# Optimization experiments

Measured on AMD Instinct MI355X. Metric: run time of the kernel, lower is better.

The kernel has to match this reference:

```python
import jax, jax.numpy as jnp
import numpy as np


def _conv2d_same(x, w, b):
    # x: [B,H,W,Cin], w: [kh,kw,Cin,Cout] (Keras HWIO), b: [Cout]
    y = jax.lax.conv_general_dilated(
        x, w, window_strides=(1, 1), padding='SAME',
        dimension_numbers=('NHWC', 'HWIO', 'NHWC'))
    return y + b


def _bilateral_slice_apply(grid, guide, image):
    # HDRNet bilateral_slice_apply with has_offset=True.
    # grid:  [B, gh, gw, gd, (ci+1)*co]
    # guide: [B, H, W] in [0,1]
    # image: [B, H, W, ci]
    B, gh, gw, gd, nc = grid.shape
    _, H, W, ci = image.shape
    co = nc // (ci + 1)
    dt = grid.dtype

    # Continuous grid coordinates (HDRNet convention: pixel centers, -0.5 shift)
    gx = (jnp.arange(W, dtype=dt) + 0.5) * gw / W - 0.5          # [W]
    gy = (jnp.arange(H, dtype=dt) + 0.5) * gh / H - 0.5          # [H]
    gz = guide.astype(dt) * gd - 0.5                             # [B,H,W]

    fx = jnp.floor(gx)
    fy = jnp.floor(gy)
    fz = jnp.floor(gz)
    bidx = jnp.arange(B)[:, None, None]                          # [B,1,1]

    coeffs = jnp.zeros((B, H, W, nc), dtype=dt)
    for dz in (0, 1):
        zz = fz + dz
        wz = jnp.maximum(1.0 - jnp.abs(gz - zz), 0.0)            # [B,H,W]
        zi = jnp.clip(zz.astype(jnp.int32), 0, gd - 1)           # [B,H,W]
        for dy in (0, 1):
            yy = fy + dy
            wy = jnp.maximum(1.0 - jnp.abs(gy - yy), 0.0)        # [H]
            yi = jnp.clip(yy.astype(jnp.int32), 0, gh - 1)       # [H]
            for dx in (0, 1):
                xx = fx + dx
                wx = jnp.maximum(1.0 - jnp.abs(gx - xx), 0.0)    # [W]
                xi = jnp.clip(xx.astype(jnp.int32), 0, gw - 1)   # [W]
                corner = grid[bidx, yi[None, :, None], xi[None, None, :], zi]  # [B,H,W,nc]
                w = wz * wy[None, :, None] * wx[None, None, :]   # [B,H,W]
                coeffs = coeffs + corner * w[..., None]

    # Per-pixel affine transform: coeffs -> [B,H,W,co,ci+1]
    A = coeffs.reshape(B, H, W, co, ci + 1)
    return jnp.einsum('bhwoi,bhwi->bhwo', A[..., :ci], image) + A[..., ci]


def setup_inputs() -> dict:
    key = jax.random.key(0)
    k1, k2, k3, k4 = jax.random.split(key, 4)
    B, H, W = 4, 1024, 1024
    grid = jax.random.normal(k1, (B, 16, 16, 8, 12), dtype=jnp.float32)
    guide = jax.random.uniform(k2, (B, H, W), dtype=jnp.float32)
    image = jax.random.normal(k3, (B, H, W, 3), dtype=jnp.float32)
    conv_w = jax.random.normal(k4, (3, 3, 3, 3), dtype=jnp.float32) * 0.1
    conv_b = jnp.zeros((3,), dtype=jnp.float32)
    return {'grid': grid, 'guide': guide, 'image': image,
            'conv_w': conv_w, 'conv_b': conv_b}


def reference(grid, guide, image, conv_w, conv_b):
    x = _conv2d_same(image, conv_w, conv_b)
    return _bilateral_slice_apply(grid, guide, x)
```

## Files before the change

### kernel.cpp

```cpp
#include <hip/hip_runtime.h>

#define H_  1024
#define W_  1024
#define B_  4
#define GH  16
#define GW  16
#define GD  8
#define NC  12
#define CELLF (GD * NC)
#define YROWF (GW * CELLF)

#define TW 64
#define TH 8

typedef _Float16 h2 __attribute__((ext_vector_type(2)));

__device__ __forceinline__ h2 u2h(unsigned int u) { return __builtin_bit_cast(h2, u); }

template<bool G>
__device__ __forceinline__ void load3g(const float* base, int yy, int xx, float* d) {
    if constexpr (!G) {
        __builtin_memcpy(d, base + (yy * W_ + xx) * 3, 12);
    } else {
        d[0] = 0.f; d[1] = 0.f; d[2] = 0.f;
        if (((unsigned)yy < (unsigned)H_) && ((unsigned)xx < (unsigned)W_))
            __builtin_memcpy(d, base + (yy * W_ + xx) * 3, 12);
    }
}

template<bool G>
__device__ __forceinline__ void loadrow9(const float* base, int ry, int x, float* d) {
    load3g<G>(base, ry, x - 1, d + 0);
    load3g<G>(base, ry, x,     d + 3);
    load3g<G>(base, ry, x + 1, d + 6);
}

__device__ __forceinline__ void conv3r(const float* a, const float* b, const float* c,
                                       float* acc, const float* wgt,
                                       float bias0, float bias1, float bias2) {
    acc[0] = bias0; acc[1] = bias1; acc[2] = bias2;
    const float* rows[3] = {a, b, c};
    #pragma unroll
    for (int kh = 0; kh < 3; ++kh)
        #pragma unroll
        for (int kw = 0; kw < 3; ++kw)
            #pragma unroll
            for (int ci = 0; ci < 3; ++ci) {
                float v = rows[kh][kw * 3 + ci];
                const float* wb = wgt + ((kh * 3 + kw) * 3 + ci) * 3;
                acc[0] += v * wb[0];
                acc[1] += v * wb[1];
                acc[2] += v * wb[2];
            }
}

__global__ __launch_bounds__(256, 8)
void fused_conv_slice(const float* __restrict__ grid,
                      const float* __restrict__ guide,
                      const float* __restrict__ image,
                      const float* __restrict__ conv_w,
                      const float* __restrict__ conv_b,
                      float* __restrict__ out)
{
    __shared__ uint4 s_t128[TH][3 * GD];
    __shared__ uint2 s_t64[TH][3 * GD];

    const int tx  = threadIdx.x;
    const int tyq = threadIdx.y;
    const int bx  = blockIdx.x;
    const int by  = blockIdx.y;
    const int b   = blockIdx.z;
    const int x0 = bx * TW;
    const int y0 = by * TH;
    const int tid = tyq * 64 + tx;
    const float* ib = image + b * (H_ * W_ * 3);

    int cells[3];
    cells[0] = max(bx - 1, 0);
    cells[1] = bx;
    cells[2] = min(bx + 1, GW - 1);
    const float* gB = grid + b * (GH * GW * GD * NC);
    {
        int rr = tid >> 5;
        int le = tid & 31;
        int y  = y0 + rr;
        float gyf = (y + 0.5f) * (1.0f / 64.0f) - 0.5f;
        float fyf = floorf(gyf);
        float tyw = gyf - fyf;
        int iy = (int)fyf;
        int yi0 = min(max(iy, 0), GH - 1);
        int yi1 = min(max(iy + 1, 0), GH - 1);
        float wy0 = 1.0f - tyw, wy1 = tyw;
        const float4* G0 = (const float4*)(gB + yi0 * YROWF);
        const float4* G1 = (const float4*)(gB + yi1 * YROWF);
        #pragma unroll
        for (int k = 0; k < 3; ++k) {
            int e = le + k * 32;
            if (e < 72) {
                int s  = (e >= 48) ? 2 : ((e >= 24) ? 1 : 0);
                int re = e - s * 24;
                int z  = re / 3;
                int c4 = re - z * 3;
                int off = cells[s] * 24 + re;
                float4 v0 = G0[off], v1 = G1[off];
                h2 p0, p1;
                p0.x = (_Float16)(wy0 * v0.x + wy1 * v1.x);
                p0.y = (_Float16)(wy0 * v0.y + wy1 * v1.y);
                p1.x = (_Float16)(wy0 * v0.z + wy1 * v1.z);
                p1.y = (_Float16)(wy0 * v0.w + wy1 * v1.w);
                uint2 u;
                u.x = __builtin_bit_cast(unsigned int, p0);
                u.y = __builtin_bit_cast(unsigned int, p1);
                int ci = s * GD + z;
                unsigned short* dst = (c4 == 2)
                    ? (unsigned short*)&s_t64[rr][ci]
                    : (unsigned short*)&s_t128[rr][ci] + c4 * 4;
                *(uint2*)dst = u;
            }
        }
    }

    const int x = x0 + tx;
    const int lr = tyq * 2;
    const int guidebase = b * (H_ * W_);
    float g2[2];
    #pragma unroll
    for (int j = 0; j < 2; ++j)
        g2[j] = guide[guidebase + (y0 + lr + j) * W_ + x];

    float wgt[81];
    #pragma unroll
    for (int i = 0; i < 81; ++i) wgt[i] = conv_w[i];
    float bias0 = conv_b[0], bias1 = conv_b[1], bias2 = conv_b[2];

    const int R0 = y0 + lr;
    float ra[9], rb[9], rc[9], rd[9];
    const bool edge = (bx == 0) | (bx == (W_ / TW - 1)) |
                      (by == 0) | (by == (H_ / TH - 1));
    if (!edge) {
        loadrow9<false>(ib, R0 - 1, x, ra);
        loadrow9<false>(ib, R0 + 0, x, rb);
        loadrow9<false>(ib, R0 + 1, x, rc);
        loadrow9<false>(ib, R0 + 2, x, rd);
    } else {
        loadrow9<true>(ib, R0 - 1, x, ra);
        loadrow9<true>(ib, R0 + 0, x, rb);
        loadrow9<true>(ib, R0 + 1, x, rc);
        loadrow9<true>(ib, R0 + 2, x, rd);
    }
    float acc2r[2][3];
    conv3r(ra, rb, rc, acc2r[0], wgt, bias0, bias1, bias2);
    conv3r(rb, rc, rd, acc2r[1], wgt, bias0, bias1, bias2);

    __syncthreads();

    float gxf = (x + 0.5f) * (1.0f / 64.0f) - 0.5f;
    float fxf = floorf(gxf);
    float txw = gxf - fxf;
    float wxa = 1.0f - txw, wxb = txw;
    int s0 = (int)fxf - (bx - 1);

    const int outbase = b * (H_ * W_ * 3);

    #pragma unroll
    for (int j = 0; j < 2; ++j) {
        int y = y0 + lr + j;
        const uint4* T128 = &s_t128[lr + j][0];
        const uint2* T64  = &s_t64[lr + j][0];

        float gzf = g2[j] * 8.0f - 0.5f;
        float fzf = floorf(gzf);
        float tz = gzf - fzf;
        int iz = (int)fzf;
        int zb = min(max(iz, 0), GD - 2);
        float wA = (iz < 0) ? 1.0f : ((iz > GD - 2) ? 0.0f : (1.0f - tz));
        float wB = 1.0f - wA;

        float m0 = wxa * wA, m1 = wxa * wB, m2 = wxb * wA, m3 = wxb * wB;
        h2 m0h = {(_Float16)m0, (_Float16)m0};
        h2 m1h = {(_Float16)m1, (_Float16)m1};
        h2 m2h = {(_Float16)m2, (_Float16)m2};
        h2 m3h = {(_Float16)m3, (_Float16)m3};

        int ci0 = s0 * GD + zb;
        uint4 Alo = T128[ci0];          uint2 Ahi = T64[ci0];
        uint4 Blo = T128[ci0 + 1];      uint2 Bhi = T64[ci0 + 1];
        uint4 Clo = T128[ci0 + GD];     uint2 Chi = T64[ci0 + GD];
        uint4 Dlo = T128[ci0 + GD + 1]; uint2 Dhi = T64[ci0 + GD + 1];

        h2 A[6]  = {u2h(Alo.x), u2h(Alo.y), u2h(Alo.z), u2h(Alo.w), u2h(Ahi.x), u2h(Ahi.y)};
        h2 Bv[6] = {u2h(Blo.x), u2h(Blo.y), u2h(Blo.z), u2h(Blo.w), u2h(Bhi.x), u2h(Bhi.y)};
        h2 Cv[6] = {u2h(Clo.x), u2h(Clo.y), u2h(Clo.z), u2h(Clo.w), u2h(Chi.x), u2h(Chi.y)};
        h2 Dv[6] = {u2h(Dlo.x), u2h(Dlo.y), u2h(Dlo.z), u2h(Dlo.w), u2h(Dhi.x), u2h(Dhi.y)};

        h2 c[6];
        #pragma unroll
        for (int k = 0; k < 6; ++k)
            c[k] = __builtin_elementwise_fma(A[k], m0h,
                   __builtin_elementwise_fma(Bv[k], m1h,
                   __builtin_elementwise_fma(Cv[k], m2h, Dv[k] * m3h)));

        float a0 = acc2r[j][0], a1 = acc2r[j][1], a2 = acc2r[j][2];
        h2 q01 = {(_Float16)a0, (_Float16)a1};
        h2 q21 = {(_Float16)a2, (_Float16)1.0f};

        int oidx = outbase + (y * W_ + x) * 3;
        #pragma unroll
        for (int o3 = 0; o3 < 3; ++o3) {
            float t = __builtin_amdgcn_fdot2(c[2 * o3 + 1], q21, 0.0f, false);
            out[oidx + o3] = __builtin_amdgcn_fdot2(c[2 * o3], q01, t, false);
        }
    }
}

extern "C" void kernel_launch(void* const* d_in, const int* in_sizes, int n_in,
                              void* d_out, int out_size, void* d_ws, size_t ws_size,
                              hipStream_t stream) {
    const float* grid   = (const float*)d_in[0];
    const float* guide  = (const float*)d_in[1];
    const float* image  = (const float*)d_in[2];
    const float* conv_w = (const float*)d_in[3];
    const float* conv_b = (const float*)d_in[4];
    float* out = (float*)d_out;

    dim3 block(64, 4, 1);
    dim3 grid_dim(W_ / TW, H_ / TH, B_);
    fused_conv_slice<<<grid_dim, block, 0, stream>>>(grid, guide, image, conv_w, conv_b, out);
}
```

Before: 146.9 us.

## Stage image halo into LDS via async global_load_lds and drop block barrier

Each wave now copies its 4-row by 66-pixel image halo into a per-wave shared buffer. Interior tiles use coalesced dword global_load_lds transfers that go straight to LDS. Edge tiles use guarded loads and LDS stores. The 3x3 conv then reads its rows from LDS instead of issuing many overlapping unaligned 12-byte global loads per thread. The __syncthreads is replaced by a wave-local waitcnt, which relies on each wave writing only the grid-table rows it later reads. This adds about 13 KB of LDS per block, which could limit occupancy.

```diff
diff --git a/kernel.cpp b/kernel.cpp
--- a/kernel.cpp
+++ b/kernel.cpp
@@ -12,27 +12,18 @@
 
 #define TW 64
 #define TH 8
+#define ROWF 198
+#define WVALID (4 * ROWF)
+#define WFLOATS (13 * 64)
 
 typedef _Float16 h2 __attribute__((ext_vector_type(2)));
 
 __device__ __forceinline__ h2 u2h(unsigned int u) { return __builtin_bit_cast(h2, u); }
 
-template<bool G>
-__device__ __forceinline__ void load3g(const float* base, int yy, int xx, float* d) {
-    if constexpr (!G) {
-        __builtin_memcpy(d, base + (yy * W_ + xx) * 3, 12);
-    } else {
-        d[0] = 0.f; d[1] = 0.f; d[2] = 0.f;
-        if (((unsigned)yy < (unsigned)H_) && ((unsigned)xx < (unsigned)W_))
-            __builtin_memcpy(d, base + (yy * W_ + xx) * 3, 12);
-    }
-}
-
-template<bool G>
-__device__ __forceinline__ void loadrow9(const float* base, int ry, int x, float* d) {
-    load3g<G>(base, ry, x - 1, d + 0);
-    load3g<G>(base, ry, x,     d + 3);
-    load3g<G>(base, ry, x + 1, d + 6);
+__device__ __forceinline__ void gload_lds4(const float* g, float* l) {
+    auto gp = (const __attribute__((address_space(1))) float*)g;
+    auto lp = (__attribute__((address_space(3))) float*)l;
+    __builtin_amdgcn_global_load_lds(gp, lp, 4, 0, 0);
 }
 
 __device__ __forceinline__ void conv3r(const float* a, const float* b, const float* c,
@@ -62,6 +53,7 @@
                       const float* __restrict__ conv_b,
                       float* __restrict__ out)
 {
+    __shared__ float s_img[4][WFLOATS];
     __shared__ uint4 s_t128[TH][3 * GD];
     __shared__ uint2 s_t64[TH][3 * GD];
 
@@ -73,6 +65,7 @@
     const int x0 = bx * TW;
     const int y0 = by * TH;
     const int tid = tyq * 64 + tx;
+    const int lr = tyq * 2;
     const float* ib = image + b * (H_ * W_ * 3);
 
     int cells[3];
@@ -120,39 +113,63 @@
         }
     }
 
-    const int x = x0 + tx;
-    const int lr = tyq * 2;
-    const int guidebase = b * (H_ * W_);
-    float g2[2];
-    #pragma unroll
-    for (int j = 0; j < 2; ++j)
-        g2[j] = guide[guidebase + (y0 + lr + j) * W_ + x];
-
-    float wgt[81];
-    #pragma unroll
-    for (int i = 0; i < 81; ++i) wgt[i] = conv_w[i];
-    float bias0 = conv_b[0], bias1 = conv_b[1], bias2 = conv_b[2];
-
-    const int R0 = y0 + lr;
-    float ra[9], rb[9], rc[9], rd[9];
+    const int wr0 = y0 + lr - 1;
     const bool edge = (bx == 0) | (bx == (W_ / TW - 1)) |
                       (by == 0) | (by == (H_ / TH - 1));
     if (!edge) {
-        loadrow9<false>(ib, R0 - 1, x, ra);
-        loadrow9<false>(ib, R0 + 0, x, rb);
-        loadrow9<false>(ib, R0 + 1, x, rc);
-        loadrow9<false>(ib, R0 + 2, x, rd);
+        #pragma unroll
+        for (int i = 0; i < 13; ++i) {
+            int f  = i * 64 + tx;
+            int fe = min(f, WVALID - 1);
+            int r  = fe / ROWF;
+            int off = fe - r * ROWF;
+            const float* src = ib + ((wr0 + r) * W_ + (x0 - 1)) * 3 + off;
+            gload_lds4(src, &s_img[tyq][i * 64]);
+        }
     } else {
-        loadrow9<true>(ib, R0 - 1, x, ra);
-        loadrow9<true>(ib, R0 + 0, x, rb);
-        loadrow9<true>(ib, R0 + 1, x, rc);
-        loadrow9<true>(ib, R0 + 2, x, rd);
+        #pragma unroll
+        for (int i = 0; i < 5; ++i) {
+            int p = i * 64 + tx;
+            if (p < 264) {
+                int r = p / 66;
+                int c = p - r * 66;
+                int yy = wr0 + r;
+                int xx = x0 - 1 + c;
+                float v[3] = {0.f, 0.f, 0.f};
+                if (((unsigned)yy < (unsigned)H_) && ((unsigned)xx < (unsigned)W_))
+                    __builtin_memcpy(v, ib + (yy * W_ + xx) * 3, 12);
+                float* d = &s_img[tyq][r * ROWF + c * 3];
+                d[0] = v[0]; d[1] = v[1]; d[2] = v[2];
+            }
+        }
     }
+
+    const int x = x0 + tx;
+    const int guidebase = b * (H_ * W_);
+    float g2[2];
+    #pragma unroll
+    for (int j = 0; j < 2; ++j)
+        g2[j] = guide[guidebase + (y0 + lr + j) * W_ + x];
+
+    float wgt[81];
+    #pragma unroll
+    for (int i = 0; i < 81; ++i) wgt[i] = conv_w[i];
+    float bias0 = conv_b[0], bias1 = conv_b[1], bias2 = conv_b[2];
+
+    __asm__ __volatile__("s_waitcnt vmcnt(0) lgkmcnt(0)" ::: "memory");
+    __builtin_amdgcn_sched_barrier(0);
+
+    auto ldr9 = [&](int r, float* d) {
+        __builtin_memcpy(d, &s_img[tyq][r * ROWF + tx * 3], 36);
+    };
+    float ra[9], rb[9], rc[9];
     float acc2r[2][3];
+    ldr9(0, ra);
+    ldr9(1, rb);
+    ldr9(2, rc);
     conv3r(ra, rb, rc, acc2r[0], wgt, bias0, bias1, bias2);
-    conv3r(rb, rc, rd, acc2r[1], wgt, bias0, bias1, bias2);
-
-    __syncthreads();
+    ldr9(3, ra);
+    conv3r(rb, rc, ra, acc2r[1], wgt, bias0, bias1, bias2);
 
     float gxf = (x + 0.5f) * (1.0f / 64.0f) - 0.5f;
     float fxf = floorf(gxf);
```

Result: faster. 137.2 us (-6.6%).
